# Performance work log

Hardware: AMD Instinct MI355X
Metric: run time of the kernel (lower is better)

## Reference

```python
import jax, jax.numpy as jnp
import numpy as np

B, T, L = 16, 2048, 512
CH, H_ENC, H_DEC, ATTN_SZ, VOCAB, EMB = 256, 100, 200, 50, 6, 64


def _conv1d(x, k):
    # x: [B,T,Cin], k: [K,Cin,Cout], SAME padding, stride 1
    return jax.lax.conv_general_dilated(x, k, (1,), 'SAME', dimension_numbers=('NWC', 'WIO', 'NWC'))


def _lstm_step(x, c, h, W, b):
    # TF BasicLSTMCell: gates ordered [i, j, f, o], forget_bias = 1.0
    z = jnp.concatenate([x, h], -1) @ W + b
    i, j, f, o = jnp.split(z, 4, -1)
    nc = c * jax.nn.sigmoid(f + 1.0) + jax.nn.sigmoid(i) * jnp.tanh(j)
    nh = jnp.tanh(nc) * jax.nn.sigmoid(o)
    return nc, nh


def _run_lstm(xs, lengths, W, b, hidden):
    # dynamic_rnn semantics: beyond sequence_length, state held, output zeroed
    Bn, Tn, _ = xs.shape
    mask = (jnp.arange(Tn)[:, None] < lengths[None, :])[..., None]  # [T,B,1]

    def step(carry, inp):
        c, h = carry
        x, m = inp
        nc, nh = _lstm_step(x, c, h, W, b)
        c = jnp.where(m, nc, c)
        h = jnp.where(m, nh, h)
        return (c, h), jnp.where(m, nh, 0.0)

    init = (jnp.zeros((Bn, hidden), xs.dtype), jnp.zeros((Bn, hidden), xs.dtype))
    (c, h), outs = jax.lax.scan(step, init, (jnp.swapaxes(xs, 0, 1), mask))
    return jnp.swapaxes(outs, 0, 1), c, h


def _reverse_seq(x, lengths):
    # tf.reverse_sequence along time axis
    t = jnp.arange(x.shape[1])[None, :]
    idx = jnp.where(t < lengths[:, None], lengths[:, None] - 1 - t, t)
    return jnp.take_along_axis(x, idx[..., None], axis=1)


def setup_inputs():
    key = jax.random.key(0)
    ks = jax.random.split(key, 16)
    s = 0.05
    f32 = jnp.float32
    return {
        'signals': jax.random.normal(ks[0], (B, T), f32),
        'embeddings': jax.random.normal(ks[1], (VOCAB, EMB), f32) * s,
        'conv1_k': jax.random.normal(ks[2], (1, 1, CH), f32) * s,
        'conv1a_k': jax.random.normal(ks[3], (1, 1, CH), f32) * s,
        'conv1a_b': jnp.zeros((CH,), f32),
        'conv2_k': jax.random.normal(ks[4], (3, CH, CH), f32) * s,
        'conv3_k': jax.random.normal(ks[5], (1, CH, CH), f32) * s,
        'W_fwd': jax.random.normal(ks[6], (CH + H_ENC, 4 * H_ENC), f32) * s,
        'b_fwd': jnp.zeros((4 * H_ENC,), f32),
        'W_bwd': jax.random.normal(ks[7], (CH + H_ENC, 4 * H_ENC), f32) * s,
        'b_bwd': jnp.zeros((4 * H_ENC,), f32),
        'W_dec': jax.random.normal(ks[8], (EMB + ATTN_SZ + H_DEC, 4 * H_DEC), f32) * s,
        'b_dec': jnp.zeros((4 * H_DEC,), f32),
        'W_mem': jax.random.normal(ks[9], (H_DEC, H_DEC), f32) * s,
        'W_attn': jax.random.normal(ks[10], (2 * H_DEC, ATTN_SZ), f32) * s,
        'W_out': jax.random.normal(ks[11], (ATTN_SZ, VOCAB), f32) * s,
        'labels': jax.random.randint(ks[12], (B, L), 0, 4),
        'sig_length': jax.random.randint(ks[13], (B,), T // 2, T + 1),
        'base_length': jax.random.randint(ks[14], (B,), L // 2, L + 1),
    }


def reference(signals, embeddings, conv1_k, conv1a_k, conv1a_b, conv2_k, conv3_k,
              W_fwd, b_fwd, W_bwd, b_bwd, W_dec, b_dec, W_mem, W_attn, W_out,
              labels, sig_length, base_length):
    # ---- resBlock ----
    x = signals[..., None]                       # [B,T,1]
    c1 = _conv1d(x, conv1_k)                     # no bias
    c1a = _conv1d(x, conv1a_k) + conv1a_b        # with bias (shortcut)
    c3 = _conv1d(_conv1d(c1, conv2_k), conv3_k)
    feat = jax.nn.relu(c3 + c1a)                 # [B,T,256]

    # ---- bidirectional encoder ----
    fwd_out, cf, hf = _run_lstm(feat, sig_length, W_fwd, b_fwd, H_ENC)
    bwd_out, cb, hb = _run_lstm(_reverse_seq(feat, sig_length), sig_length, W_bwd, b_bwd, H_ENC)
    bwd_out = _reverse_seq(bwd_out, sig_length)
    memory = jnp.concatenate([fwd_out, bwd_out], -1)   # [B,T,200]
    c0 = jnp.concatenate([cf, cb], -1)                 # [B,200]
    h0 = jnp.concatenate([hf, hb], -1)

    # ---- Luong attention decoder (teacher forcing) ----
    keys = jnp.einsum('btd,de->bte', memory, W_mem)    # memory_layer (no bias)
    mem_mask = jnp.arange(T)[None, :] < sig_length[:, None]
    neg = jnp.finfo(memory.dtype).min
    emb = embeddings[labels]                            # [B,L,64]

    def dec_step(carry, x_t):
        c, h, attn = carry
        nc, nh = _lstm_step(jnp.concatenate([x_t, attn], -1), c, h, W_dec, b_dec)
        score = jnp.einsum('bd,btd->bt', nh, keys)
        align = jax.nn.softmax(jnp.where(mem_mask, score, neg), axis=-1)
        ctx = jnp.einsum('bt,btd->bd', align, memory)
        new_attn = jnp.concatenate([nh, ctx], -1) @ W_attn   # attention_layer (no bias)
        return (nc, nh, new_attn), new_attn @ W_out          # output Dense(6, no bias)

    attn0 = jnp.zeros((B, ATTN_SZ), memory.dtype)
    _, logits = jax.lax.scan(dec_step, (c0, h0, attn0), jnp.swapaxes(emb, 0, 1))
    logits = jnp.swapaxes(logits, 0, 1)                      # [B,L,6]
    dec_mask = (jnp.arange(L)[None, :] < base_length[:, None])[..., None]
    return jnp.where(dec_mask, logits, jnp.zeros((), logits.dtype))
```

## Files before the change

### kernel.cpp

```cpp
#include <hip/hip_runtime.h>

#define B_ 16
#define T_ 2048
#define L_ 512
#define HD 200
#define AT 50

__device__ __forceinline__ float rcp_(float x){ return __builtin_amdgcn_rcpf(x); }
__device__ __forceinline__ float sigf(float x){ return rcp_(1.f + __expf(-x)); }
__device__ __forceinline__ float tanhf_(float x){
  x = fminf(15.f, fmaxf(-15.f, x));
  float e = __expf(-2.f*x);
  return (1.f - e) * rcp_(1.f + e);
}
__device__ __forceinline__ unsigned bf16u(float v){
  unsigned u = __float_as_uint(v);
  u += 0x7FFFu + ((u >> 16) & 1u);
  return u >> 16;
}
__device__ __forceinline__ unsigned long long pkvs(float v, unsigned s){
  return (unsigned long long)__float_as_uint(v) | ((unsigned long long)s << 32);
}

__global__ void k_prep(const float* __restrict__ conv1, const float* __restrict__ conv1a,
                       const float* __restrict__ conv2, const float* __restrict__ conv3,
                       float* __restrict__ E)
{
  __shared__ float K2s[3*256];
  int tid = threadIdx.x;
  int k = tid >> 8, co = tid & 255;
  float a = 0.f;
  for (int ci = 0; ci < 256; ++ci)
    a = fmaf(conv1[ci], conv2[(k*256 + ci)*256 + co], a);
  K2s[k*256 + co] = a;
  __syncthreads();
  float b2 = 0.f;
  for (int ci = 0; ci < 256; ++ci)
    b2 = fmaf(K2s[k*256 + ci], conv3[ci*256 + co], b2);
  if (k == 1) b2 += conv1a[co];
  E[k*256 + co] = b2;
}

__global__ void k_feat(const float* __restrict__ sig, const float* __restrict__ E,
                       const float* __restrict__ c1ab, float* __restrict__ feat)
{
  int idx = blockIdx.x*256 + threadIdx.x;
  int row = idx >> 6;
  int c4  = (idx & 63) * 4;
  int t = row & (T_-1);
  float sm = (t > 0)     ? sig[row-1] : 0.f;
  float s0 = sig[row];
  float sp = (t < T_-1)  ? sig[row+1] : 0.f;
  float4 e0 = *(const float4*)&E[0*256 + c4];
  float4 e1 = *(const float4*)&E[1*256 + c4];
  float4 e2 = *(const float4*)&E[2*256 + c4];
  float4 bb = *(const float4*)&c1ab[c4];
  float4 r;
  r.x = fmaxf(0.f, fmaf(sm, e0.x, fmaf(s0, e1.x, fmaf(sp, e2.x, bb.x))));
  r.y = fmaxf(0.f, fmaf(sm, e0.y, fmaf(s0, e1.y, fmaf(sp, e2.y, bb.y))));
  r.z = fmaxf(0.f, fmaf(sm, e0.z, fmaf(s0, e1.z, fmaf(sp, e2.z, bb.z))));
  r.w = fmaxf(0.f, fmaf(sm, e0.w, fmaf(s0, e1.w, fmaf(sp, e2.w, bb.w))));
  *(float4*)&feat[(size_t)row*256 + c4] = r;
}

__global__ __launch_bounds__(256)
void k_gemm(const float* __restrict__ A, const float* __restrict__ B,
            const float* __restrict__ bias, float* __restrict__ C,
            int M, int N, int K, int ldb)
{
  __shared__ float As[16][132];
  __shared__ float Bs[16][68];
  int row0 = blockIdx.x*128, col0 = blockIdx.y*64;
  int tid = threadIdx.x;
  int tm = tid >> 4, tn = tid & 15;
  float acc[8][4] = {};
  for (int k0 = 0; k0 < K; k0 += 16){
    #pragma unroll
    for (int i = 0; i < 8; ++i){
      int e = tid + i*256;
      int m = e >> 4, kk = e & 15;
      float v = 0.f;
      if (k0 + kk < K) v = A[(size_t)(row0+m)*K + k0 + kk];
      As[kk][m] = v;
    }
    #pragma unroll
    for (int i = 0; i < 4; ++i){
      int e = tid + i*256;
      int n = e & 63, kb = e >> 6;
      float w = 0.f;
      if (k0 + kb < K && col0 + n < N) w = B[(size_t)(k0+kb)*ldb + col0 + n];
      Bs[kb][n] = w;
    }
    __syncthreads();
    #pragma unroll
    for (int kk = 0; kk < 16; ++kk){
      float a[8], bv[4];
      *(float4*)&a[0] = *(const float4*)&As[kk][tm*8];
      *(float4*)&a[4] = *(const float4*)&As[kk][tm*8+4];
      *(float4*)&bv[0] = *(const float4*)&Bs[kk][tn*4];
      #pragma unroll
      for (int i = 0; i < 8; ++i)
        #pragma unroll
        for (int j = 0; j < 4; ++j)
          acc[i][j] = fmaf(a[i], bv[j], acc[i][j]);
    }
    __syncthreads();
  }
  #pragma unroll
  for (int i = 0; i < 8; ++i){
    int r = row0 + tm*8 + i;
    #pragma unroll
    for (int j = 0; j < 4; ++j){
      int cc = col0 + tn*4 + j;
      if (cc < N) C[(size_t)r*N + cc] = acc[i][j] + (bias ? bias[cc] : 0.f);
    }
  }
}

__global__ void k_permW(const float* __restrict__ Wf, const float* __restrict__ bf,
                        const float* __restrict__ Wb, const float* __restrict__ bb,
                        float* __restrict__ WpF, float* __restrict__ WpB)
{
  int idx = blockIdx.x*256 + threadIdx.x;
  if (idx >= 2*357*400) return;
  int w = idx / (357*400), r = idx - w*(357*400);
  int j = r / 400, col = r - j*400;
  int src = (col & 3)*100 + (col >> 2);
  const float* W = w ? Wb : Wf; const float* bs = w ? bb : bf;
  float v = (j < 356) ? W[j*400 + src] : bs[src];
  (w ? WpB : WpF)[j*400 + col] = v;
}

__global__ __launch_bounds__(512, 1)
void k_encoder(const float* __restrict__ xprojF, const float* __restrict__ xprojB,
               const float* __restrict__ WpF, const float* __restrict__ WpB,
               const int* __restrict__ sig_len, float* __restrict__ memory,
               float* __restrict__ c0h0, int dirParam)
{
  int dir = dirParam, b = blockIdx.x;
  const float* xp = dir ? xprojB : xprojF;
  const float* Wp = dir ? WpB : WpF;
  int tid = threadIdx.x;
  bool act = tid < 400;
  int col = act ? tid : (tid - 400);
  int u = tid >> 2, gq = tid & 3;
  __shared__ __align__(16) float h2[2][104];
  float4 Uv[25];
  #pragma unroll
  for (int j4 = 0; j4 < 25; ++j4){
    Uv[j4].x = Wp[(256 + 4*j4 + 0)*400 + col];
    Uv[j4].y = Wp[(256 + 4*j4 + 1)*400 + col];
    Uv[j4].z = Wp[(256 + 4*j4 + 2)*400 + col];
    Uv[j4].w = Wp[(256 + 4*j4 + 3)*400 + col];
  }
  if (tid < 100) h2[0][tid] = 0.f;
  int len = sig_len[b];
  float c = 0.f, hfin = 0.f;
  int ta = dir ? (len-1) : 0;
  float xb0 = xp[((size_t)(b*T_ + ta))*400 + col];
  int tb_ = dir ? (len-2) : 1;
  float xb1 = xp[((size_t)(b*T_ + tb_))*400 + col];
  for (int step = 0; step < len; ++step){
    __syncthreads();
    int tn = dir ? (len-3-step) : (step+2);
    tn = tn < 0 ? 0 : (tn > T_-1 ? T_-1 : tn);
    float xn = xp[((size_t)(b*T_ + tn))*400 + col];
    const float* hb = h2[step & 1];
    float a0 = xb0, a1 = 0.f, a2 = 0.f, a3 = 0.f;
    #pragma unroll
    for (int j4 = 0; j4 < 25; ++j4){
      float4 h4 = *(const float4*)&hb[j4*4];
      a0 = fmaf(h4.x, Uv[j4].x, a0);
      a1 = fmaf(h4.y, Uv[j4].y, a1);
      a2 = fmaf(h4.z, Uv[j4].z, a2);
      a3 = fmaf(h4.w, Uv[j4].w, a3);
    }
    float z = (a0+a1)+(a2+a3);
    float v0 = z, v1 = __shfl_xor(z, 1);
    float v2 = __shfl_xor(v0, 2), v3 = __shfl_xor(v1, 2);
    float tA  = (gq&1) ? v1 : v0, tB  = (gq&1) ? v3 : v2;
    float tA2 = (gq&1) ? v0 : v1, tB2 = (gq&1) ? v2 : v3;
    float zi = (gq&2) ? tB  : tA;
    float zj = (gq&2) ? tB2 : tA2;
    float zf = (gq&2) ? tA  : tB;
    float zo = (gq&2) ? tA2 : tB2;
    c = c*sigf(zf + 1.f) + sigf(zi)*tanhf_(zj);
    float nh = tanhf_(c)*sigf(zo);
    hfin = nh;
    if (act && gq == 0){
      int t = dir ? (len-1-step) : step;
      h2[(step+1)&1][u] = nh;
      memory[((size_t)(b*T_ + t))*200 + dir*100 + u] = nh;
    }
    xb0 = xb1; xb1 = xn;
  }
  if (act && gq == 0){
    c0h0[b*400 + dir*100 + u]       = c;
    c0h0[b*400 + 200 + dir*100 + u] = hfin;
  }
  int total = (T_ - len)*100;
  for (int i = tid; i < total; i += 512){
    int t = len + i/100;
    int k = i - (i/100)*100;
    memory[((size_t)(b*T_ + t))*200 + dir*100 + k] = 0.f;
  }
}

__global__ void k_gather(const float* __restrict__ emb, const int* __restrict__ labels,
                         float* __restrict__ dA)
{
  int idx = blockIdx.x*256 + threadIdx.x;
  int i = idx >> 6, e = idx & 63;
  dA[(size_t)i*64 + e] = emb[labels[i]*64 + e];
}

__global__ void k_dec_init(unsigned long long* __restrict__ nhb,
                           unsigned long long* __restrict__ parts,
                           unsigned* __restrict__ flags, unsigned fval,
                           float* __restrict__ out)
{
  int idx = blockIdx.x*256 + threadIdx.x;
  if (idx < B_*L_*6) out[idx] = 0.f;
  if (idx < B_*HD) nhb[idx] = 0ull;
  if (idx < B_*16*112) parts[idx] = 0ull;
  if (idx < 32) flags[idx] = fval;
}

#define DEC_LDS 137728
#define TCH 128

__global__ __launch_bounds__(256, 1)
void k_fused(const float* __restrict__ xprojF, const float* __restrict__ xprojB,
             const float* __restrict__ WpF, const float* __restrict__ WpB,
             float* __restrict__ memG, float* c0h0,
             const float* __restrict__ W_mem, const float* __restrict__ W_attn,
             const float* __restrict__ decx, const float* __restrict__ W_dec,
             const float* __restrict__ W_out,
             const int* __restrict__ sig_len, const int* __restrict__ base_len,
             unsigned long long* nhb, unsigned long long* partials,
             unsigned* flags, int encInside,
             float* __restrict__ out)
{
  int blk = blockIdx.x;
  int b = (blk & 7) | (((blk >> 3) & 1) << 3);
  int g = blk >> 4;
  int tid = threadIdx.x;
  int u0 = g * 13;
  int nu = (HD - u0 < 13) ? (HD - u0) : 13;
  int t0 = g * TCH;

  extern __shared__ char smem[];
  uint2* keyP  = (uint2*)(smem);
  float* memAL = (float*)(smem + 51616);
  float* Uld   = (float*)(smem + 77216);
  float* Wa1s  = (float*)(smem + 129216);
  float* WoutL = (float*)(smem + 131824);
  float* nhF   = (float*)(smem + 133024);
  float* spL   = (float*)(smem + 133856);
  float* wL    = (float*)(smem + 134880);
  float* cpL   = (float*)(smem + 135392);
  float* apL   = (float*)(smem + 136016);
  float* zp    = (float*)(smem + 136224);
  float* attnL = (float*)(smem + 137056);
  float* SL    = (float*)(smem + 137264);
  float* ctxR  = (float*)(smem + 137272);
  float* apR   = (float*)(smem + 137480);

  if (encInside && g < 2){
    int dir = g;
    const float* xp = dir ? xprojB : xprojF;
    const float* Wp = dir ? WpB : WpF;
    float* h2 = spL;
    int col2 = (tid < 144) ? (256 + tid) : 256;
    float4 U1[25], U2[25];
    #pragma unroll
    for (int j4 = 0; j4 < 25; ++j4){
      U1[j4].x = Wp[(256 + 4*j4 + 0)*400 + tid];
      U1[j4].y = Wp[(256 + 4*j4 + 1)*400 + tid];
      U1[j4].z = Wp[(256 + 4*j4 + 2)*400 + tid];
      U1[j4].w = Wp[(256 + 4*j4 + 3)*400 + tid];
      U2[j4].x = Wp[(256 + 4*j4 + 0)*400 + col2];
      U2[j4].y = Wp[(256 + 4*j4 + 1)*400 + col2];
      U2[j4].z = Wp[(256 + 4*j4 + 2)*400 + col2];
      U2[j4].w = Wp[(256 + 4*j4 + 3)*400 + col2];
    }
    if (tid < 104) h2[tid] = 0.f;
    int len = sig_len[b];
    int u1 = tid >> 2, gq = tid & 3;
    int u2 = 64 + u1;
    float c1 = 0.f, c2 = 0.f, hf1 = 0.f, hf2 = 0.f;
    int taa = dir ? (len-1) : 0;
    int tbb = dir ? (len-2) : 1;
    float xA0 = xp[((size_t)(b*T_ + taa))*400 + tid];
    float xB0 = xp[((size_t)(b*T_ + taa))*400 + col2];
    float xA1 = xp[((size_t)(b*T_ + tbb))*400 + tid];
    float xB1 = xp[((size_t)(b*T_ + tbb))*400 + col2];
    for (int step = 0; step < len; ++step){
      __syncthreads();
      int tn = dir ? (len-3-step) : (step+2);
      tn = tn < 0 ? 0 : (tn > T_-1 ? T_-1 : tn);
      float xA2 = xp[((size_t)(b*T_ + tn))*400 + tid];
      float xB2 = xp[((size_t)(b*T_ + tn))*400 + col2];
      const float* hb = h2 + (step & 1)*104;
      float a0 = xA0, a1 = 0.f, a2 = 0.f, a3 = 0.f;
      float b0 = xB0, b1 = 0.f, b2 = 0.f, b3 = 0.f;
      #pragma unroll
      for (int j4 = 0; j4 < 25; ++j4){
        float4 h4 = *(const float4*)&hb[j4*4];
        a0 = fmaf(h4.x, U1[j4].x, a0);
        a1 = fmaf(h4.y, U1[j4].y, a1);
        a2 = fmaf(h4.z, U1[j4].z, a2);
        a3 = fmaf(h4.w, U1[j4].w, a3);
        b0 = fmaf(h4.x, U2[j4].x, b0);
        b1 = fmaf(h4.y, U2[j4].y, b1);
        b2 = fmaf(h4.z, U2[j4].z, b2);
        b3 = fmaf(h4.w, U2[j4].w, b3);
      }
      float z1 = (a0+a1)+(a2+a3);
      float z2 = (b0+b1)+(b2+b3);
      float v0 = z1, v1 = __shfl_xor(z1, 1);
      float v2 = __shfl_xor(v0, 2), v3 = __shfl_xor(v1, 2);
      float w0 = z2, w1 = __shfl_xor(z2, 1);
      float w2 = __shfl_xor(w0, 2), w3 = __shfl_xor(w1, 2);
      float tA, tB, tA2v, tB2v, zi, zj, zf, zo;
      tA  = (gq&1) ? v1 : v0; tB  = (gq&1) ? v3 : v2;
      tA2v = (gq&1) ? v0 : v1; tB2v = (gq&1) ? v2 : v3;
      zi = (gq&2) ? tB : tA;  zj = (gq&2) ? tB2v : tA2v;
      zf = (gq&2) ? tA : tB;  zo = (gq&2) ? tA2v : tB2v;
      c1 = c1*sigf(zf + 1.f) + sigf(zi)*tanhf_(zj);
      float nh1 = tanhf_(c1)*sigf(zo);
      hf1 = nh1;
      tA  = (gq&1) ? w1 : w0; tB  = (gq&1) ? w3 : w2;
      tA2v = (gq&1) ? w0 : w1; tB2v = (gq&1) ? w2 : w3;
      zi = (gq&2) ? tB : tA;  zj = (gq&2) ? tB2v : tA2v;
      zf = (gq&2) ? tA : tB;  zo = (gq&2) ? tA2v : tB2v;
      c2 = c2*sigf(zf + 1.f) + sigf(zi)*tanhf_(zj);
      float nh2 = tanhf_(c2)*sigf(zo);
      hf2 = nh2;
      float* hn = h2 + ((step+1)&1)*104;
      if (gq == 0){
        int t = dir ? (len-1-step) : step;
        hn[u1] = nh1;
        memG[((size_t)(b*T_ + t))*200 + dir*100 + u1] = nh1;
        if (tid < 144){
          hn[u2] = nh2;
          memG[((size_t)(b*T_ + t))*200 + dir*100 + u2] = nh2;
        }
      }
      xA0 = xA1; xA1 = xA2; xB0 = xB1; xB1 = xB2;
    }
    if ((tid & 3) == 0){
      int u1w = tid >> 2;
      c0h0[b*400 + dir*100 + u1w]       = c1;
      c0h0[b*400 + 200 + dir*100 + u1w] = hf1;
      if (tid < 144){
        c0h0[b*400 + dir*100 + 64 + u1w]       = c2;
        c0h0[b*400 + 200 + dir*100 + 64 + u1w] = hf2;
      }
    }
    int total = (T_ - len)*100;
    for (int i = tid; i < total; i += 256){
      int t = len + i/100;
      int k = i - (i/100)*100;
      memG[((size_t)(b*T_ + t))*200 + dir*100 + k] = 0.f;
    }
    __syncthreads();
    if (tid == 0){
      __builtin_amdgcn_fence(__ATOMIC_RELEASE, "agent");
      __hip_atomic_store(&flags[b*2 + dir], 1u,
                         __ATOMIC_RELAXED, __HIP_MEMORY_SCOPE_AGENT);
    }
  }

  if (encInside){
    if (tid == 0){
      while (__hip_atomic_load(&flags[b*2+0], __ATOMIC_RELAXED, __HIP_MEMORY_SCOPE_AGENT) == 0u)
        __builtin_amdgcn_s_sleep(8);
      while (__hip_atomic_load(&flags[b*2+1], __ATOMIC_RELAXED, __HIP_MEMORY_SCOPE_AGENT) == 0u)
        __builtin_amdgcn_s_sleep(8);
      __builtin_amdgcn_fence(__ATOMIC_ACQUIRE, "agent");
    }
    __syncthreads();
  }

  unsigned* stg = (unsigned*)Uld;
  for (int i = tid; i < TCH*100; i += 256){
    int t = i / 100, p2 = i - (i/100)*100;
    float2 mv = *(const float2*)&memG[((size_t)(b*T_ + t0 + t))*200 + 2*p2];
    stg[i] = bf16u(mv.x) | (bf16u(mv.y) << 16);
  }
  __syncthreads();
  {
    int t = tid >> 1, dh = tid & 1;
    const unsigned* mrow = stg + t*100;
    for (int dq = 0; dq < 25; ++dq){
      int d = dh*100 + dq*4;
      float ax = 0.f, ay = 0.f, az = 0.f, aw = 0.f;
      for (int p2 = 0; p2 < 100; ++p2){
        unsigned mm = mrow[p2];
        float m0 = __uint_as_float(mm << 16);
        float m1 = __uint_as_float(mm & 0xFFFF0000u);
        float4 w0 = *(const float4*)&W_mem[(size_t)(2*p2)*200 + d];
        float4 w1 = *(const float4*)&W_mem[(size_t)(2*p2+1)*200 + d];
        ax = fmaf(m0, w0.x, fmaf(m1, w1.x, ax));
        ay = fmaf(m0, w0.y, fmaf(m1, w1.y, ay));
        az = fmaf(m0, w0.z, fmaf(m1, w1.z, az));
        aw = fmaf(m0, w0.w, fmaf(m1, w1.w, aw));
      }
      keyP[(d>>2)*129 + t] = make_uint2(bf16u(ax) | (bf16u(ay) << 16),
                                        bf16u(az) | (bf16u(aw) << 16));
    }
    for (int dd = 0; dd < 25; ++dd){
      int d = dh*25 + dd;
      float acc = 0.f;
      for (int p2 = 0; p2 < 100; ++p2){
        unsigned mm = mrow[p2];
        float m0 = __uint_as_float(mm << 16);
        float m1 = __uint_as_float(mm & 0xFFFF0000u);
        acc = fmaf(m0, W_attn[(size_t)(200 + 2*p2)*50 + d],
              fmaf(m1, W_attn[(size_t)(201 + 2*p2)*50 + d], acc));
      }
      memAL[t*50 + d] = acc;
    }
  }
  __syncthreads();

  for (int i = tid; i < 250*52; i += 256){
    int j = i / 52, o_ = i - (i/52)*52;
    int uu = o_ >> 2, gg = o_ & 3;
    Uld[i] = (uu < nu) ? W_dec[(size_t)(64 + j)*800 + gg*200 + u0 + uu] : 0.f;
  }
  for (int i = tid; i < 13*50; i += 256){
    int uu = i / 50, d = i - (i/50)*50;
    Wa1s[i] = (uu < nu) ? W_attn[(size_t)(u0 + uu)*50 + d] : 0.f;
  }
  for (int i = tid; i < 300; i += 256) WoutL[i] = W_out[i];
  if (tid < 50) attnL[tid] = 0.f;
  if (tid < 8)  nhF[200 + tid] = 0.f;
  float creg = (tid < nu) ? c0h0[b*400 + u0 + tid] : 0.f;
  int len = sig_len[b];
  int Lb  = base_len[b];
  unsigned long long* nhB = nhb + (size_t)b*HD;
  __syncthreads();

  if (tid < 50) *(float4*)&nhF[tid*4] = *(const float4*)&c0h0[b*400 + 200 + tid*4];
  __syncthreads();
  int o  = tid - (tid/52)*52;
  int jc = tid / 52;
  float zh = 0.f, dcx = 0.f;
  if (tid < 208){
    const float* Ub = &Uld[(50 + jc*50)*52 + o];
    const float* hp = &nhF[jc*50];
    #pragma unroll 10
    for (int j = 0; j < 50; ++j) zh = fmaf(hp[j], Ub[(size_t)j*52], zh);
    if (jc == 0) dcx = decx[((size_t)(b*L_))*800 + (o&3)*200 + u0 + (o>>2)];
  }

  for (int l = 0; l < Lb; ++l){
    unsigned seq = (unsigned)(l + 1);
    if (tid < 208){
      float z = zh + ((jc == 0) ? dcx : 0.f);
      const float* Ub = &Uld[(jc*13)*52 + o];
      const float* ap_ = &attnL[jc*13];
      int cnt = (jc < 3) ? 13 : 11;
      for (int j = 0; j < cnt; ++j) z = fmaf(ap_[j], Ub[(size_t)j*52], z);
      zp[o*4 + jc] = z;
    } else if (g == 1 && l > 0 && tid < 214){
      int j = tid - 208;
      float o_ = 0.f;
      for (int d = 0; d < AT; ++d) o_ = fmaf(attnL[d], WoutL[d*6 + j], o_);
      out[((size_t)(b*L_ + (l-1)))*6 + j] = o_;
    }
    __syncthreads();
    if (tid < nu){
      const float* zz = &zp[(4*tid)*4];
      float zi = (zz[0]+zz[1])+(zz[2]+zz[3]);
      float zj = (zz[4]+zz[5])+(zz[6]+zz[7]);
      float zf = (zz[8]+zz[9])+(zz[10]+zz[11]);
      float zo = (zz[12]+zz[13])+(zz[14]+zz[15]);
      float c = creg;
      c = c*sigf(zf + 1.f) + sigf(zi)*tanhf_(zj);
      creg = c;
      float nh = tanhf_(c)*sigf(zo);
      __hip_atomic_store(&nhB[u0 + tid], pkvs(nh, seq),
                         __ATOMIC_RELAXED, __HIP_MEMORY_SCOPE_AGENT);
    }
    if (tid < HD){
      unsigned long long v;
      do {
        v = __hip_atomic_load(&nhB[tid], __ATOMIC_RELAXED, __HIP_MEMORY_SCOPE_AGENT);
      } while ((unsigned)(v >> 32) != seq);
      nhF[tid] = __uint_as_float((unsigned)v);
    }
    __syncthreads();
    {
      int t = tid & 127, dh = tid >> 7;
      const uint2* kp = &keyP[(dh*25)*129 + t];
      const float4* nf = (const float4*)nhF + dh*25;
      float s0 = 0.f, s1 = 0.f;
      #pragma unroll
      for (int q = 0; q < 25; ++q){
        uint2 kk = kp[(size_t)q*129];
        float4 nv = nf[q];
        s0 = fmaf(nv.x, __uint_as_float(kk.x << 16), s0);
        s1 = fmaf(nv.y, __uint_as_float(kk.x & 0xFFFF0000u), s1);
        s0 = fmaf(nv.z, __uint_as_float(kk.y << 16), s0);
        s1 = fmaf(nv.w, __uint_as_float(kk.y & 0xFFFF0000u), s1);
      }
      spL[tid] = s0 + s1;
    }
    __syncthreads();
    if (tid < 128){
      float s = spL[tid] + spL[tid + 128];
      float w = 0.f;
      if (t0 + tid < len){ s = fminf(60.f, fmaxf(-60.f, s)); w = __expf(s); }
      wL[tid] = w;
    } else if (tid < 178){
      int d = tid - 128;
      float a = 0.f;
      #pragma unroll
      for (int uu = 0; uu < 13; ++uu) a = fmaf(nhF[u0 + uu], Wa1s[uu*50 + d], a);
      apL[d] = a;
    }
    __syncthreads();
    if (tid >= 192){
      float v = wL[tid - 192] + wL[tid - 128];
      #pragma unroll
      for (int off = 32; off > 0; off >>= 1) v += __shfl_down(v, off);
      if (tid == 192) SL[0] = v;
    } else {
      int tc = tid >> 6, d = tid & 63;
      if (d < 50){
        int tlo = tc*43, thi = (tc == 2) ? 128 : tc*43 + 43;
        float a = 0.f;
        for (int t = tlo; t < thi; ++t) a = fmaf(wL[t], memAL[t*50 + d], a);
        cpL[tc*52 + d] = a;
      }
    }
    __syncthreads();
    {
      unsigned long long* pb = partials + (size_t)(b*16 + g)*112;
      if (tid < 50)
        __hip_atomic_store(&pb[tid],
                           pkvs((cpL[tid] + cpL[52 + tid]) + cpL[104 + tid], seq),
                           __ATOMIC_RELAXED, __HIP_MEMORY_SCOPE_AGENT);
      else if (tid < 100)
        __hip_atomic_store(&pb[tid], pkvs(apL[tid - 50], seq),
                           __ATOMIC_RELAXED, __HIP_MEMORY_SCOPE_AGENT);
      else if (tid == 100)
        __hip_atomic_store(&pb[100], pkvs(SL[0], seq),
                           __ATOMIC_RELAXED, __HIP_MEMORY_SCOPE_AGENT);
    }
    zh = 0.f;
    if (tid < 208){
      const float* Ub = &Uld[(50 + jc*50)*52 + o];
      const float* hp = &nhF[jc*50];
      #pragma unroll 10
      for (int j = 0; j < 50; ++j) zh = fmaf(hp[j], Ub[(size_t)j*52], zh);
      if (jc == 0 && l+1 < Lb)
        dcx = decx[((size_t)(b*L_ + (l+1)))*800 + (o&3)*200 + u0 + (o>>2)];
    }
    if (tid < 101){
      const unsigned long long* base = partials + (size_t)b*16*112 + tid;
      unsigned long long v[16];
      #pragma unroll
      for (int gg = 0; gg < 16; ++gg)
        v[gg] = __hip_atomic_load(&base[gg*112], __ATOMIC_RELAXED, __HIP_MEMORY_SCOPE_AGENT);
      #pragma unroll
      for (int gg = 0; gg < 16; ++gg)
        while ((unsigned)(v[gg] >> 32) != seq)
          v[gg] = __hip_atomic_load(&base[gg*112], __ATOMIC_RELAXED, __HIP_MEMORY_SCOPE_AGENT);
      float acc = 0.f;
      #pragma unroll
      for (int gg = 0; gg < 16; ++gg) acc += __uint_as_float((unsigned)v[gg]);
      if (tid < 50) ctxR[tid] = acc;
      else if (tid < 100) apR[tid - 50] = acc;
      else SL[1] = acc;
    }
    __syncthreads();
    if (tid < 50) attnL[tid] = fmaf(ctxR[tid], rcp_(SL[1]), apR[tid]);
    __syncthreads();
  }
  if (g == 1 && tid < 6){
    float o_ = 0.f;
    for (int d = 0; d < AT; ++d) o_ = fmaf(attnL[d], WoutL[d*6 + tid], o_);
    out[((size_t)(b*L_ + (Lb-1)))*6 + tid] = o_;
  }
}

extern "C" void kernel_launch(void* const* d_in, const int* in_sizes, int n_in,
                              void* d_out, int out_size, void* d_ws, size_t ws_size,
                              hipStream_t stream)
{
  const float* signals   = (const float*)d_in[0];
  const float* embeddings= (const float*)d_in[1];
  const float* conv1_k   = (const float*)d_in[2];
  const float* conv1a_k  = (const float*)d_in[3];
  const float* conv1a_b  = (const float*)d_in[4];
  const float* conv2_k   = (const float*)d_in[5];
  const float* conv3_k   = (const float*)d_in[6];
  const float* W_fwd     = (const float*)d_in[7];
  const float* b_fwd     = (const float*)d_in[8];
  const float* W_bwd     = (const float*)d_in[9];
  const float* b_bwd     = (const float*)d_in[10];
  const float* W_dec     = (const float*)d_in[11];
  const float* b_dec     = (const float*)d_in[12];
  const float* W_mem     = (const float*)d_in[13];
  const float* W_attn    = (const float*)d_in[14];
  const float* W_out     = (const float*)d_in[15];
  const int*   labels    = (const int*)d_in[16];
  const int*   sig_len   = (const int*)d_in[17];
  const int*   base_len  = (const int*)d_in[18];
  float* out = (float*)d_out;
  char* ws = (char*)d_ws;

  const size_t o_c0h0     = 4096;
  const size_t o_nhbuf    = 32768;
  const size_t o_partials = 65536;
  const size_t o_flags    = 458752;
  const size_t o_WpF      = 589824;
  const size_t o_WpB      = 1161024;
  const size_t o_feat     = 4194304;
  const size_t o_mem      = o_feat + 33554432;
  const size_t o_X1       = o_mem + 26214400;
  const size_t o_X2       = o_X1 + 52428800;

  bool bigws = (ws_size >= o_X2 + 52428800);

  float* E      = (float*)(ws);
  float* c0h0   = (float*)(ws + o_c0h0);
  unsigned long long* nhbuf = (unsigned long long*)(ws + o_nhbuf);
  unsigned long long* parts = (unsigned long long*)(ws + o_partials);
  unsigned* flags = (unsigned*)(ws + o_flags);
  float* WpF    = (float*)(ws + o_WpF);
  float* WpB    = (float*)(ws + o_WpB);
  float* feat   = (float*)(ws + o_feat);
  float* memory = (float*)(ws + o_mem);
  float* xprojF = (float*)(ws + o_X1);
  float* xprojB = bigws ? (float*)(ws + o_X2) : xprojF;
  float* decxA  = (float*)(ws + o_feat);
  float* decx   = (float*)(ws + o_feat + 4194304);

  k_prep<<<1, 768, 0, stream>>>(conv1_k, conv1a_k, conv2_k, conv3_k, E);
  k_feat<<<8192, 256, 0, stream>>>(signals, E, conv1a_b, feat);
  k_permW<<<1116, 256, 0, stream>>>(W_fwd, b_fwd, W_bwd, b_bwd, WpF, WpB);

  dim3 gx(256, 7);
  if (bigws){
    k_gemm<<<gx, 256, 0, stream>>>(feat, WpF, WpF + 356*400, xprojF, 32768, 400, 256, 400);
    k_gemm<<<gx, 256, 0, stream>>>(feat, WpB, WpB + 356*400, xprojB, 32768, 400, 256, 400);
  } else {
    k_gemm<<<gx, 256, 0, stream>>>(feat, WpF, WpF + 356*400, xprojF, 32768, 400, 256, 400);
    k_encoder<<<16, 512, 0, stream>>>(xprojF, xprojF, WpF, WpB, sig_len, memory, c0h0, 0);
    k_gemm<<<gx, 256, 0, stream>>>(feat, WpB, WpB + 356*400, xprojF, 32768, 400, 256, 400);
    k_encoder<<<16, 512, 0, stream>>>(xprojF, xprojF, WpF, WpB, sig_len, memory, c0h0, 1);
  }

  k_gather<<<2048, 256, 0, stream>>>(embeddings, labels, decxA);
  k_gemm<<<dim3(64, 13), 256, 0, stream>>>(decxA, W_dec, b_dec, decx, 8192, 800, 64, 800);
  k_dec_init<<<192, 256, 0, stream>>>(nhbuf, parts, flags, bigws ? 0u : 1u, out);

  hipFuncSetAttribute(reinterpret_cast<const void*>(k_fused),
                      hipFuncAttributeMaxDynamicSharedMemorySize, DEC_LDS);
  k_fused<<<256, 256, DEC_LDS, stream>>>(xprojF, xprojB, WpF, WpB,
                                         memory, c0h0, W_mem, W_attn,
                                         decx, W_dec, W_out,
                                         sig_len, base_len,
                                         nhbuf, parts, flags, bigws ? 1 : 0,
                                         out);
}
```

Measured before the change: 5.110 ms.

## Keep recurrent weights in registers and broadcast hidden state via readlane

The encoder LSTM now holds its first weight set as 100 scalar registers per thread and moves the second weight set into LDS. It reads the hidden state once per lane and broadcasts it with readlane instead of issuing float4 LDS reads per FMA. The decoder moves its recurrent weights (Uh, Ua) and the attention memory slice (Mw) from LDS into registers and uses readlane broadcasts for the h, attn and softmax-weight vectors. The aim is to cut LDS traffic on the serial per-step critical path. The cost is heavy register pressure, with waves_per_eu pinned to 1, and longer serial FMA chains with no split accumulators.

New measurement: 6.328 ms. +23.8%, slower.

```diff
diff --git a/kernel.cpp b/kernel.cpp
--- a/kernel.cpp
+++ b/kernel.cpp
@@ -20,6 +20,9 @@
 }
 __device__ __forceinline__ unsigned long long pkvs(float v, unsigned s){
   return (unsigned long long)__float_as_uint(v) | ((unsigned long long)s << 32);
+}
+__device__ __forceinline__ float RL(float v, int l){
+  return __uint_as_float(__builtin_amdgcn_readlane(__float_as_uint(v), l));
 }
 
 __global__ void k_prep(const float* __restrict__ conv1, const float* __restrict__ conv1a,
@@ -229,7 +232,8 @@
 #define DEC_LDS 137728
 #define TCH 128
 
-__global__ __launch_bounds__(256, 1)
+__global__ __launch_bounds__(256)
+__attribute__((amdgpu_waves_per_eu(1, 1)))
 void k_fused(const float* __restrict__ xprojF, const float* __restrict__ xprojB,
              const float* __restrict__ WpF, const float* __restrict__ WpB,
              float* __restrict__ memG, float* c0h0,
@@ -270,92 +274,91 @@
     int dir = g;
     const float* xp = dir ? xprojB : xprojF;
     const float* Wp = dir ? WpB : WpF;
-    float* h2 = spL;
-    int col2 = (tid < 144) ? (256 + tid) : 256;
-    float4 U1[25], U2[25];
-    #pragma unroll
-    for (int j4 = 0; j4 < 25; ++j4){
-      U1[j4].x = Wp[(256 + 4*j4 + 0)*400 + tid];
-      U1[j4].y = Wp[(256 + 4*j4 + 1)*400 + tid];
-      U1[j4].z = Wp[(256 + 4*j4 + 2)*400 + tid];
-      U1[j4].w = Wp[(256 + 4*j4 + 3)*400 + tid];
-      U2[j4].x = Wp[(256 + 4*j4 + 0)*400 + col2];
-      U2[j4].y = Wp[(256 + 4*j4 + 1)*400 + col2];
-      U2[j4].z = Wp[(256 + 4*j4 + 2)*400 + col2];
-      U2[j4].w = Wp[(256 + 4*j4 + 3)*400 + col2];
-    }
-    if (tid < 104) h2[tid] = 0.f;
+    float* WL2 = (float*)smem;
+    float* h2  = spL;
+    for (int i = tid; i < 25*144*4; i += 256){
+      int j4 = i / 576, r = i - j4*576;
+      WL2[i] = Wp[(256 + 4*j4 + (r & 3))*400 + 256 + (r >> 2)];
+    }
+    h2[tid] = 0.f;
+    float U1[100];
+    #pragma unroll
+    for (int j = 0; j < 100; ++j) U1[j] = Wp[(256 + j)*400 + tid];
     int len = sig_len[b];
-    int u1 = tid >> 2, gq = tid & 3;
-    int u2 = 64 + u1;
-    float c1 = 0.f, c2 = 0.f, hf1 = 0.f, hf2 = 0.f;
+    int gq = tid & 3;
+    bool has2 = tid < 144;
+    int col2 = 256 + (has2 ? tid : 0);
+    int lane = tid & 63;
+    float c1 = 0.f, c2v = 0.f, hf1 = 0.f, hf2 = 0.f;
     int taa = dir ? (len-1) : 0;
     int tbb = dir ? (len-2) : 1;
     float xA0 = xp[((size_t)(b*T_ + taa))*400 + tid];
-    float xB0 = xp[((size_t)(b*T_ + taa))*400 + col2];
     float xA1 = xp[((size_t)(b*T_ + tbb))*400 + tid];
-    float xB1 = xp[((size_t)(b*T_ + tbb))*400 + col2];
+    float xB0 = has2 ? xp[((size_t)(b*T_ + taa))*400 + col2] : 0.f;
+    float xB1 = has2 ? xp[((size_t)(b*T_ + tbb))*400 + col2] : 0.f;
     for (int step = 0; step < len; ++step){
       __syncthreads();
       int tn = dir ? (len-3-step) : (step+2);
       tn = tn < 0 ? 0 : (tn > T_-1 ? T_-1 : tn);
       float xA2 = xp[((size_t)(b*T_ + tn))*400 + tid];
-      float xB2 = xp[((size_t)(b*T_ + tn))*400 + col2];
-      const float* hb = h2 + (step & 1)*104;
-      float a0 = xA0, a1 = 0.f, a2 = 0.f, a3 = 0.f;
-      float b0 = xB0, b1 = 0.f, b2 = 0.f, b3 = 0.f;
-      #pragma unroll
-      for (int j4 = 0; j4 < 25; ++j4){
-        float4 h4 = *(const float4*)&hb[j4*4];
-        a0 = fmaf(h4.x, U1[j4].x, a0);
-        a1 = fmaf(h4.y, U1[j4].y, a1);
-        a2 = fmaf(h4.z, U1[j4].z, a2);
-        a3 = fmaf(h4.w, U1[j4].w, a3);
-        b0 = fmaf(h4.x, U2[j4].x, b0);
-        b1 = fmaf(h4.y, U2[j4].y, b1);
-        b2 = fmaf(h4.z, U2[j4].z, b2);
-        b3 = fmaf(h4.w, U2[j4].w, b3);
+      float xB2 = has2 ? xp[((size_t)(b*T_ + tn))*400 + col2] : 0.f;
+      const float* hb = h2 + (step & 1)*128;
+      float hr0 = hb[lane];
+      float hr1 = hb[64 + lane];
+      float z1 = xA0;
+      #pragma unroll
+      for (int j = 0; j < 100; ++j)
+        z1 = fmaf((j < 64) ? RL(hr0, j) : RL(hr1, j - 64), U1[j], z1);
+      float z2 = xB0;
+      if (has2){
+        #pragma unroll
+        for (int j4 = 0; j4 < 25; ++j4){
+          float4 w2 = *(const float4*)&WL2[(j4*144 + tid)*4];
+          int j = j4*4;
+          z2 = fmaf((j   < 64) ? RL(hr0, j  ) : RL(hr1, j-64),   w2.x, z2);
+          z2 = fmaf((j+1 < 64) ? RL(hr0, j+1) : RL(hr1, j-63),   w2.y, z2);
+          z2 = fmaf((j+2 < 64) ? RL(hr0, j+2) : RL(hr1, j-62),   w2.z, z2);
+          z2 = fmaf((j+3 < 64) ? RL(hr0, j+3) : RL(hr1, j-61),   w2.w, z2);
+        }
       }
-      float z1 = (a0+a1)+(a2+a3);
-      float z2 = (b0+b1)+(b2+b3);
       float v0 = z1, v1 = __shfl_xor(z1, 1);
       float v2 = __shfl_xor(v0, 2), v3 = __shfl_xor(v1, 2);
-      float w0 = z2, w1 = __shfl_xor(z2, 1);
-      float w2 = __shfl_xor(w0, 2), w3 = __shfl_xor(w1, 2);
-      float tA, tB, tA2v, tB2v, zi, zj, zf, zo;
-      tA  = (gq&1) ? v1 : v0; tB  = (gq&1) ? v3 : v2;
-      tA2v = (gq&1) ? v0 : v1; tB2v = (gq&1) ? v2 : v3;
-      zi = (gq&2) ? tB : tA;  zj = (gq&2) ? tB2v : tA2v;
-      zf = (gq&2) ? tA : tB;  zo = (gq&2) ? tA2v : tB2v;
+      float tA  = (gq&1) ? v1 : v0, tB  = (gq&1) ? v3 : v2;
+      float tA2 = (gq&1) ? v0 : v1, tB2 = (gq&1) ? v2 : v3;
+      float zi = (gq&2) ? tB : tA,  zj = (gq&2) ? tB2 : tA2;
+      float zf = (gq&2) ? tA : tB,  zo = (gq&2) ? tA2 : tB2;
       c1 = c1*sigf(zf + 1.f) + sigf(zi)*tanhf_(zj);
       float nh1 = tanhf_(c1)*sigf(zo);
       hf1 = nh1;
-      tA  = (gq&1) ? w1 : w0; tB  = (gq&1) ? w3 : w2;
-      tA2v = (gq&1) ? w0 : w1; tB2v = (gq&1) ? w2 : w3;
-      zi = (gq&2) ? tB : tA;  zj = (gq&2) ? tB2v : tA2v;
-      zf = (gq&2) ? tA : tB;  zo = (gq&2) ? tA2v : tB2v;
-      c2 = c2*sigf(zf + 1.f) + sigf(zi)*tanhf_(zj);
-      float nh2 = tanhf_(c2)*sigf(zo);
+      float w0 = z2, w1 = __shfl_xor(z2, 1);
+      float w2s = __shfl_xor(w0, 2), w3 = __shfl_xor(w1, 2);
+      tA  = (gq&1) ? w1 : w0;  tB  = (gq&1) ? w3 : w2s;
+      tA2 = (gq&1) ? w0 : w1;  tB2 = (gq&1) ? w2s : w3;
+      zi = (gq&2) ? tB : tA;   zj = (gq&2) ? tB2 : tA2;
+      zf = (gq&2) ? tA : tB;   zo = (gq&2) ? tA2 : tB2;
+      c2v = c2v*sigf(zf + 1.f) + sigf(zi)*tanhf_(zj);
+      float nh2 = tanhf_(c2v)*sigf(zo);
       hf2 = nh2;
-      float* hn = h2 + ((step+1)&1)*104;
+      float* hn = h2 + ((step+1)&1)*128;
       if (gq == 0){
         int t = dir ? (len-1-step) : step;
+        int u1 = tid >> 2;
         hn[u1] = nh1;
         memG[((size_t)(b*T_ + t))*200 + dir*100 + u1] = nh1;
-        if (tid < 144){
-          hn[u2] = nh2;
-          memG[((size_t)(b*T_ + t))*200 + dir*100 + u2] = nh2;
+        if (has2){
+          hn[64 + u1] = nh2;
+          memG[((size_t)(b*T_ + t))*200 + dir*100 + 64 + u1] = nh2;
         }
       }
       xA0 = xA1; xA1 = xA2; xB0 = xB1; xB1 = xB2;
     }
     if ((tid & 3) == 0){
-      int u1w = tid >> 2;
-      c0h0[b*400 + dir*100 + u1w]       = c1;
-      c0h0[b*400 + 200 + dir*100 + u1w] = hf1;
-      if (tid < 144){
-        c0h0[b*400 + dir*100 + 64 + u1w]       = c2;
-        c0h0[b*400 + 200 + dir*100 + 64 + u1w] = hf2;
+      int u1 = tid >> 2;
+      c0h0[b*400 + dir*100 + u1]       = c1;
+      c0h0[b*400 + 200 + dir*100 + u1] = hf1;
+      if (has2){
+        c0h0[b*400 + dir*100 + 64 + u1]       = c2v;
+        c0h0[b*400 + 200 + dir*100 + 64 + u1] = hf2;
       }
     }
     int total = (T_ - len)*100;
@@ -423,19 +426,29 @@
       memAL[t*50 + d] = acc;
     }
   }
-  __syncthreads();
-
-  for (int i = tid; i < 250*52; i += 256){
-    int j = i / 52, o_ = i - (i/52)*52;
-    int uu = o_ >> 2, gg = o_ & 3;
-    Uld[i] = (uu < nu) ? W_dec[(size_t)(64 + j)*800 + gg*200 + u0 + uu] : 0.f;
+
+  int oL = tid & 63;
+  int jc = tid >> 6;
+  int uu = oL >> 2, gg = oL & 3;
+  bool vOK = (oL < 52) && (uu < nu);
+  int uuC = (uu < nu ? uu : 0);
+  float Uh[50], Ua[13];
+  #pragma unroll
+  for (int j = 0; j < 50; ++j){
+    float v = W_dec[(size_t)(114 + jc*50 + j)*800 + gg*200 + u0 + uuC];
+    Uh[j] = vOK ? v : 0.f;
+  }
+  #pragma unroll
+  for (int j = 0; j < 13; ++j){
+    float v = W_dec[(size_t)(64 + jc*13 + j)*800 + gg*200 + u0 + uuC];
+    Ua[j] = vOK ? v : 0.f;
   }
   for (int i = tid; i < 13*50; i += 256){
-    int uu = i / 50, d = i - (i/50)*50;
-    Wa1s[i] = (uu < nu) ? W_attn[(size_t)(u0 + uu)*50 + d] : 0.f;
+    int uw = i / 50, d = i - (i/50)*50;
+    Wa1s[i] = (uw < nu) ? W_attn[(size_t)(u0 + uw)*50 + d] : 0.f;
   }
   for (int i = tid; i < 300; i += 256) WoutL[i] = W_out[i];
-  if (tid < 50) attnL[tid] = 0.f;
+  if (tid < 52) attnL[tid] = 0.f;
   if (tid < 8)  nhF[200 + tid] = 0.f;
   float creg = (tid < nu) ? c0h0[b*400 + u0 + tid] : 0.f;
   int len = sig_len[b];
@@ -443,30 +456,38 @@
   unsigned long long* nhB = nhb + (size_t)b*HD;
   __syncthreads();
 
+  float Mw[43];
+  {
+    int dF = (oL < 50) ? oL : 49;
+    #pragma unroll
+    for (int i = 0; i < 43; ++i){
+      int t = jc*43 + i;
+      float v = memAL[((t < 128) ? t : 127)*50 + dF];
+      Mw[i] = (t < 128) ? v : 0.f;
+    }
+  }
+
   if (tid < 50) *(float4*)&nhF[tid*4] = *(const float4*)&c0h0[b*400 + 200 + tid*4];
   __syncthreads();
-  int o  = tid - (tid/52)*52;
-  int jc = tid / 52;
   float zh = 0.f, dcx = 0.f;
-  if (tid < 208){
-    const float* Ub = &Uld[(50 + jc*50)*52 + o];
-    const float* hp = &nhF[jc*50];
-    #pragma unroll 10
-    for (int j = 0; j < 50; ++j) zh = fmaf(hp[j], Ub[(size_t)j*52], zh);
-    if (jc == 0) dcx = decx[((size_t)(b*L_))*800 + (o&3)*200 + u0 + (o>>2)];
+  {
+    float hrg = nhF[jc*50 + oL];
+    #pragma unroll
+    for (int j = 0; j < 50; ++j) zh = fmaf(RL(hrg, j), Uh[j], zh);
+    if (jc == 0 && oL < 52)
+      dcx = decx[((size_t)(b*L_))*800 + (oL&3)*200 + u0 + (oL>>2)];
   }
 
   for (int l = 0; l < Lb; ++l){
     unsigned seq = (unsigned)(l + 1);
-    if (tid < 208){
+    if (oL < 52){
+      float ar = attnL[jc*13 + oL];
       float z = zh + ((jc == 0) ? dcx : 0.f);
-      const float* Ub = &Uld[(jc*13)*52 + o];
-      const float* ap_ = &attnL[jc*13];
-      int cnt = (jc < 3) ? 13 : 11;
-      for (int j = 0; j < cnt; ++j) z = fmaf(ap_[j], Ub[(size_t)j*52], z);
-      zp[o*4 + jc] = z;
-    } else if (g == 1 && l > 0 && tid < 214){
-      int j = tid - 208;
+      #pragma unroll
+      for (int j = 0; j < 13; ++j) z = fmaf(RL(ar, j), Ua[j], z);
+      zp[oL*4 + jc] = z;
+    } else if (g == 1 && l > 0 && tid >= 52 && tid < 58){
+      int j = tid - 52;
       float o_ = 0.f;
       for (int d = 0; d < AT; ++d) o_ = fmaf(attnL[d], WoutL[d*6 + j], o_);
       out[((size_t)(b*L_ + (l-1)))*6 + j] = o_;
@@ -519,7 +540,7 @@
       int d = tid - 128;
       float a = 0.f;
       #pragma unroll
-      for (int uu = 0; uu < 13; ++uu) a = fmaf(nhF[u0 + uu], Wa1s[uu*50 + d], a);
+      for (int uw = 0; uw < 13; ++uw) a = fmaf(nhF[u0 + uw], Wa1s[uw*50 + d], a);
       apL[d] = a;
     }
     __syncthreads();
@@ -529,13 +550,11 @@
       for (int off = 32; off > 0; off >>= 1) v += __shfl_down(v, off);
       if (tid == 192) SL[0] = v;
     } else {
-      int tc = tid >> 6, d = tid & 63;
-      if (d < 50){
-        int tlo = tc*43, thi = (tc == 2) ? 128 : tc*43 + 43;
-        float a = 0.f;
-        for (int t = tlo; t < thi; ++t) a = fmaf(wL[t], memAL[t*50 + d], a);
-        cpL[tc*52 + d] = a;
-      }
+      float wr = wL[jc*43 + oL];
+      float a = 0.f;
+      #pragma unroll
+      for (int i = 0; i < 43; ++i) a = fmaf(RL(wr, i), Mw[i], a);
+      if (oL < 50) cpL[jc*52 + oL] = a;
     }
     __syncthreads();
     {
@@ -552,27 +571,26 @@
                            __ATOMIC_RELAXED, __HIP_MEMORY_SCOPE_AGENT);
     }
     zh = 0.f;
-    if (tid < 208){
-      const float* Ub = &Uld[(50 + jc*50)*52 + o];
-      const float* hp = &nhF[jc*50];
-      #pragma unroll 10
-      for (int j = 0; j < 50; ++j) zh = fmaf(hp[j], Ub[(size_t)j*52], zh);
-      if (jc == 0 && l+1 < Lb)
-        dcx = decx[((size_t)(b*L_ + (l+1)))*800 + (o&3)*200 + u0 + (o>>2)];
+    {
+      float hrg = nhF[jc*50 + oL];
+      #pragma unroll
+      for (int j = 0; j < 50; ++j) zh = fmaf(RL(hrg, j), Uh[j], zh);
+      if (jc == 0 && oL < 52 && l+1 < Lb)
+        dcx = decx[((size_t)(b*L_ + (l+1)))*800 + (oL&3)*200 + u0 + (oL>>2)];
     }
     if (tid < 101){
       const unsigned long long* base = partials + (size_t)b*16*112 + tid;
       unsigned long long v[16];
       #pragma unroll
-      for (int gg = 0; gg < 16; ++gg)
-        v[gg] = __hip_atomic_load(&base[gg*112], __ATOMIC_RELAXED, __HIP_MEMORY_SCOPE_AGENT);
-      #pragma unroll
-      for (int gg = 0; gg < 16; ++gg)
-        while ((unsigned)(v[gg] >> 32) != seq)
-          v[gg] = __hip_atomic_load(&base[gg*112], __ATOMIC_RELAXED, __HIP_MEMORY_SCOPE_AGENT);
+      for (int gq2 = 0; gq2 < 16; ++gq2)
+        v[gq2] = __hip_atomic_load(&base[gq2*112], __ATOMIC_RELAXED, __HIP_MEMORY_SCOPE_AGENT);
+      #pragma unroll
+      for (int gq2 = 0; gq2 < 16; ++gq2)
+        while ((unsigned)(v[gq2] >> 32) != seq)
+          v[gq2] = __hip_atomic_load(&base[gq2*112], __ATOMIC_RELAXED, __HIP_MEMORY_SCOPE_AGENT);
       float acc = 0.f;
       #pragma unroll
-      for (int gg = 0; gg < 16; ++gg) acc += __uint_as_float((unsigned)v[gg]);
+      for (int gq2 = 0; gq2 < 16; ++gq2) acc += __uint_as_float((unsigned)v[gq2]);
       if (tid < 50) ctxR[tid] = acc;
       else if (tid < 100) apR[tid - 50] = acc;
       else SL[1] = acc;
```
